# Kernel tuning notes

Hardware: AMD Instinct MI355X
Metric: run time of the kernel (lower is better)

## Reference

```python
import jax, jax.numpy as jnp
import numpy as np
from jax import lax

G = 64; ELL = 0.18; VOX = ELL / G
C_VIEWS = 6; H_IMG = 256; W_IMG = 256
MAX_N = 2048; PT = 0.25; MT = 0.25; FILL = 0.45
CHUNK = 256; RADIUS_CLIP = 2.0; NEAR = 0.01


def _rotz(a):
    c, s = jnp.cos(a), jnp.sin(a)
    z = jnp.zeros_like(c); o = jnp.ones_like(c)
    return jnp.stack([jnp.stack([c, -s, z]), jnp.stack([s, c, z]), jnp.stack([z, z, o])])


def _quat_to_mat4(q):
    # faithful replication of quaternion_matrix_torch_batch (incl. its asymmetries), fp32
    eps = 4 * np.finfo(np.float32).eps
    n = jnp.sum(q * q, 1)
    qs = q * jnp.sqrt(2.0 / jnp.where(n < eps, 1.0, n))[:, None]
    o = jnp.einsum('bi,bj->bij', qs, qs)
    one = jnp.ones_like(n); zero = jnp.zeros_like(n)
    row0 = jnp.stack([1.0 - o[:, 2, 2] - o[:, 3, 3], o[:, 1, 2] - o[:, 3, 0], o[:, 1, 3] + o[:, 2, 0], zero], 1)
    row1 = jnp.stack([o[:, 1, 2] - o[:, 3, 0], one, o[:, 2, 3] - o[:, 1, 0], zero], 1)
    row2 = jnp.stack([o[:, 1, 3] - o[:, 2, 0], o[:, 2, 3] + o[:, 1, 0], 1.0 - o[:, 1, 1] - o[:, 2, 2], zero], 1)
    row3 = jnp.stack([zero, zero, zero, one], 1)
    M = jnp.stack([row0, row1, row2, row3], 1)
    return jnp.where((n < eps)[:, None, None], jnp.eye(4, dtype=q.dtype), M)


def _quat_from_mat4(m):
    m00, m01, m02 = m[:, 0, 0], m[:, 0, 1], m[:, 0, 2]
    m10, m11, m12 = m[:, 1, 0], m[:, 1, 1], m[:, 1, 2]
    m20, m21, m22 = m[:, 2, 0], m[:, 2, 1], m[:, 2, 2]
    r0 = jnp.stack([m00 - m11 - m22, m01 + m10, m02 + m20, m21 - m12], 1)
    r1 = jnp.stack([m01 + m10, m11 - m00 - m22, m12 + m21, m02 - m20], 1)
    r2 = jnp.stack([m02 + m20, m12 + m21, m22 - m00 - m11, m10 - m01], 1)
    r3 = jnp.stack([m21 - m12, m02 - m20, m10 - m01, m00 + m11 + m22], 1)
    K = jnp.stack([r0, r1, r2, r3], 1) / 3.0
    _, V = jnp.linalg.eigh(K)
    q = V[:, :, -1][:, jnp.array([3, 0, 1, 2])]
    return jnp.where(q[:, :1] < 0.0, -q, q)


def _splat(means, quats, scales, opac, colors, viewmat, K, bg):
    R3, t3 = viewmat[:3, :3], viewmat[:3, 3]
    cam = means @ R3.T + t3
    x, y, z = cam[:, 0], cam[:, 1], cam[:, 2]
    fx, fy, cx, cy = K[0, 0], K[1, 1], K[0, 2], K[1, 2]
    qn = quats / (jnp.linalg.norm(quats, axis=1, keepdims=True) + 1e-12)
    w, qx, qy, qz = qn[:, 0], qn[:, 1], qn[:, 2], qn[:, 3]
    Rq = jnp.stack([
        jnp.stack([1 - 2 * (qy * qy + qz * qz), 2 * (qx * qy - w * qz), 2 * (qx * qz + w * qy)], 1),
        jnp.stack([2 * (qx * qy + w * qz), 1 - 2 * (qx * qx + qz * qz), 2 * (qy * qz - w * qx)], 1),
        jnp.stack([2 * (qx * qz - w * qy), 2 * (qy * qz + w * qx), 1 - 2 * (qx * qx + qy * qy)], 1)], 1)
    cov3 = jnp.einsum('nij,nj,nkj->nik', Rq, scales ** 2, Rq)
    covc = jnp.einsum('ij,njk,lk->nil', R3, cov3, R3)
    rz = 1.0 / z
    zn = jnp.zeros_like(z)
    J = jnp.stack([jnp.stack([fx * rz, zn, -fx * x * rz * rz], 1),
                   jnp.stack([zn, fy * rz, -fy * y * rz * rz], 1)], 1)  # [N,2,3]
    cov2 = jnp.einsum('nij,njk,nlk->nil', J, covc, J)
    a2 = cov2[:, 0, 0] + 0.3; b2 = cov2[:, 0, 1]; c2 = cov2[:, 1, 1] + 0.3  # gsplat screen dilation
    det = a2 * c2 - b2 * b2
    det_s = jnp.where(det > 1e-12, det, 1.0)
    ca = c2 / det_s; cb = -b2 / det_s; cc = a2 / det_s  # conic
    lam = 0.5 * (a2 + c2) + jnp.sqrt(jnp.maximum(0.25 * (a2 - c2) ** 2 + b2 * b2, 1e-12))
    radius = jnp.ceil(3.0 * jnp.sqrt(lam))
    mu_x = fx * x * rz + cx; mu_y = fy * y * rz + cy
    valid = (z > NEAR) & (det > 1e-12) & (radius > RADIUS_CLIP)
    op = jnp.where(valid, opac, 0.0)
    order = jnp.argsort(z)  # front-to-back
    gac = lambda a: a[order].reshape(-1, CHUNK, *a.shape[1:])
    chunks = (gac(mu_x), gac(mu_y), gac(ca), gac(cb), gac(cc), gac(op), gac(colors))
    xs = jnp.arange(W_IMG, dtype=means.dtype) + 0.5
    ys = jnp.arange(H_IMG, dtype=means.dtype) + 0.5

    @jax.checkpoint
    def body(carry, ch):
        rgb, T = carry
        ux, uy, A, B, Cc, o_, col = ch
        dx = xs[None, None, :] - ux[:, None, None]          # [c,1,W]->[c,H,W]
        dy = ys[None, :, None] - uy[:, None, None]
        sigma = 0.5 * (A[:, None, None] * dx * dx + Cc[:, None, None] * dy * dy) + B[:, None, None] * dx * dy
        alpha = o_[:, None, None] * jnp.exp(-sigma)
        alpha = jnp.where((sigma >= 0) & (alpha >= 1.0 / 255.0), jnp.minimum(alpha, 0.999), 0.0)
        cp = jnp.cumprod(1.0 - alpha, axis=0)
        Tin = jnp.concatenate([jnp.ones_like(cp[:1]), cp[:-1]], 0)  # exclusive transmittance in chunk
        wgt = alpha * Tin * T[None]
        rgb = rgb + jnp.einsum('nhw,nc->hwc', wgt, col)
        return (rgb, T * cp[-1]), None

    init = (jnp.zeros((H_IMG, W_IMG, 3), means.dtype), jnp.ones((H_IMG, W_IMG), means.dtype))
    (rgb, T), _ = lax.scan(body, init, chunks)
    alpha_img = 1.0 - T
    rgb = jnp.clip(rgb + T[..., None] * bg, 0.0, 1.0)
    return rgb[None], alpha_img[None, :, :, None]


def _forward(mask, img, p_3d, angle, grid, Ks, viewmats, w1, b1, w2, b2, scale_param, background, view_num):
    m = mask[0]; im = img[0]
    Rz = _rotz(angle)
    # ---- shape carving: project canonical grid into all views ----
    pw = grid @ Rz.T + p_3d                                   # [V,3]
    cam = jnp.einsum('cij,vj->cvi', viewmats[:, :3, :3], pw) + viewmats[:, None, :3, 3]
    z = cam[..., 2]
    proj = jnp.einsum('cij,cvj->cvi', Ks, cam)
    u = proj[..., 0] / z; v = proj[..., 1] / z
    ui = jnp.clip(jnp.round(u).astype(jnp.int32), 0, W_IMG - 1)
    vi = jnp.clip(jnp.round(v).astype(jnp.int32), 0, H_IMG - 1)
    inb = (u >= 0) & (u < W_IMG) & (v >= 0) & (v < H_IMG) & (z > NEAR)
    cidx = jnp.arange(C_VIEWS)[:, None]
    inside = inb & (m[cidx, vi, ui] > 0.5)
    csamp = im[cidx, vi, ui]                                  # [C,V,3]
    wv = inside.astype(grid.dtype)
    frac = wv.mean(0)
    col = (wv[..., None] * csamp).sum(0) / jnp.maximum(wv.sum(0), 1.0)[:, None]
    col = jnp.where((frac >= 1.0 - 1e-6)[:, None], col, FILL)
    volume = jnp.concatenate([10.0 * frac[None] - 5.0, col.T,
                              jnp.zeros((4, grid.shape[0]), grid.dtype)], 0)  # [8, G^3] (ablation pad)
    # ---- gaussian param extraction (static top-k instead of threshold search) ----
    probs = jax.nn.sigmoid(volume[0] - MT)
    _, idx = lax.top_k(probs, MAX_N)
    feats = volume[:, idx].T                                  # [N,8]
    h = jax.nn.relu(feats @ w1 + b1)
    out = h @ w2 + b2
    quats, scl, _op, cols, dmu = jnp.split(out, [4, 7, 8, 11], axis=1)
    colors = jnp.clip(jax.nn.sigmoid(cols), 0.0, 0.99)
    scales = jnp.exp(scl + scale_param[0])
    opac = jax.nn.sigmoid(jnp.clip((probs[idx] - PT) / (1.0 - PT), 0.0, 1.0))
    means = grid[idx] + 2.0 * VOX * jnp.tanh(dmu)
    # ---- pose transform ----
    means = means @ Rz.T + p_3d
    Rz4 = jnp.eye(4, dtype=means.dtype).at[:3, :3].set(Rz)
    r = jnp.einsum('ij,bjk->bik', Rz4, _quat_to_mat4(quats))
    quats = _quat_from_mat4(r)
    return _splat(means, quats, scales, opac, colors, viewmats[view_num], Ks[view_num], background)


def setup_inputs() -> dict:
    key = jax.random.key(0)
    ks = jax.random.split(key, 6)
    mask = jax.random.uniform(ks[0], (1, C_VIEWS, H_IMG, W_IMG), jnp.float32)
    img = jax.random.uniform(ks[1], (1, C_VIEWS, H_IMG, W_IMG, 3), jnp.float32)
    p_3d = jax.random.normal(ks[2], (3,), jnp.float32) * 0.02
    angle = jax.random.uniform(ks[3], (), jnp.float32) * 2.0 * np.pi
    lin = np.linspace(-ELL / 2, ELL / 2, G, dtype=np.float32)
    gx, gy, gz = np.meshgrid(lin, lin, lin, indexing='ij')
    grid = jnp.asarray(np.stack([gx, gy, gz], -1).reshape(-1, 3))
    Kmat = np.array([[300.0, 0.0, W_IMG / 2], [0.0, 300.0, H_IMG / 2], [0.0, 0.0, 1.0]], np.float32)
    Ks = jnp.asarray(np.stack([Kmat] * C_VIEWS))
    vms = []
    up = np.array([0.0, 0.0, 1.0])
    for i in range(C_VIEWS):
        th = 2 * np.pi * i / C_VIEWS
        eye = np.array([0.8 * np.cos(th), 0.8 * np.sin(th), 0.25])
        f = -eye / np.linalg.norm(eye)
        r = np.cross(f, up); r = r / np.linalg.norm(r)
        d = np.cross(f, r)
        vm = np.eye(4, dtype=np.float32)
        vm[:3, :3] = np.stack([r, d, f]).astype(np.float32)
        vm[:3, 3] = -vm[:3, :3] @ eye.astype(np.float32)
        vms.append(vm)
    viewmats = jnp.asarray(np.stack(vms))
    w1 = jax.random.normal(ks[4], (8, 128), jnp.float32) * 0.3
    b1 = jnp.zeros((128,), jnp.float32)
    w2 = jax.random.normal(ks[5], (128, 14), jnp.float32) * 0.2
    b2 = jnp.zeros((14,), jnp.float32)
    scale_param = jnp.full((1,), -5.5, jnp.float32)
    background = jnp.ones((3,), jnp.float32)
    return dict(mask=mask, img=img, p_3d=p_3d, angle=angle, grid=grid, Ks=Ks, viewmats=viewmats,
                w1=w1, b1=b1, w2=w2, b2=b2, scale_param=scale_param, background=background, view_num=0)


def reference(mask, img, p_3d, angle, grid, Ks, viewmats, w1, b1, w2, b2, scale_param, background, view_num):
    return _forward(mask, img, p_3d, angle, grid, Ks, viewmats, w1, b1, w2, b2, scale_param, background, view_num)
```

## Files before the change

kernel.cpp:

```cpp
#include <hip/hip_runtime.h>
#include <hip/hip_bf16.h>

namespace {
constexpr int GN   = 262144;
constexpr int CV   = 6;
constexpr int HI   = 256, WI = 256;
constexpr int MAXN = 2048;
constexpr int CBLK = 256;
constexpr int NSEG = 8;
constexpr float NEARZ = 0.01f;
constexpr float FILLC = 0.45f;

constexpr size_t OFF_CNT   = 0;
constexpr size_t OFF_BC8   = OFF_CNT + GN;
constexpr size_t OFF_SEL   = OFF_BC8 + CBLK*8*4;
constexpr size_t OFF_SCNT  = OFF_SEL + MAXN*4;
constexpr size_t OFF_PAR   = OFF_SCNT + MAXN*4;
constexpr size_t OFF_KEY   = OFF_PAR + MAXN*12*4;
constexpr size_t OFF_SPAR  = OFF_KEY + MAXN*8;
constexpr size_t OFF_PART  = OFF_SPAR + MAXN*12*4;
constexpr size_t WS_NEED   = OFF_PART + (size_t)256*NSEG*256*16;
}

__device__ __forceinline__ float sigm_(float x){ return 1.0f/(1.0f+expf(-x)); }

__global__ void __launch_bounds__(1024) k_count(
    const float* __restrict__ mask, const float* __restrict__ grid,
    const float* __restrict__ p3d, const float* __restrict__ angle,
    const float* __restrict__ Ks, const float* __restrict__ vms,
    unsigned char* __restrict__ cnt8, int* __restrict__ bc8)
{
  int t = threadIdx.x;
  int p = blockIdx.x*1024 + t;
  float a = angle[0];
  float ca = cosf(a), sa = sinf(a);
  float gx = grid[p*3+0], gy = grid[p*3+1], gz = grid[p*3+2];
  float pwx = ca*gx - sa*gy + p3d[0];
  float pwy = sa*gx + ca*gy + p3d[1];
  float pwz = gz + p3d[2];
  int count = 0;
  for (int c = 0; c < CV; ++c){
    const float* R = vms + c*16;
    float cxx = R[0]*pwx + R[1]*pwy + R[2]*pwz + R[3];
    float cyy = R[4]*pwx + R[5]*pwy + R[6]*pwz + R[7];
    float czz = R[8]*pwx + R[9]*pwy + R[10]*pwz + R[11];
    const float* K = Ks + c*9;
    float u = (K[0]*cxx + K[1]*cyy + K[2]*czz)/czz;
    float v = (K[3]*cxx + K[4]*cyy + K[5]*czz)/czz;
    bool inb = (u>=0.f)&&(u<(float)WI)&&(v>=0.f)&&(v<(float)HI)&&(czz>NEARZ);
    int ui = (int)fminf(fmaxf(rintf(u),0.f),(float)(WI-1));
    int vi = (int)fminf(fmaxf(rintf(v),0.f),(float)(HI-1));
    bool inside = inb && (mask[(c*HI+vi)*WI+ui] > 0.5f);
    count += inside ? 1 : 0;
  }
  cnt8[p] = (unsigned char)count;
  __shared__ int lh[8];
  if (t < 8) lh[t] = 0;
  __syncthreads();
  int L = 6 - count;
  unsigned long long msk[7];
  #pragma unroll
  for (int lv = 0; lv < 7; ++lv) msk[lv] = __ballot(L == lv);
  int lane = t & 63;
  if (lane < 7){
    int c = (int)__popcll(msk[lane]);
    if (c) atomicAdd(&lh[lane], c);
  }
  __syncthreads();
  if (t < 8) bc8[blockIdx.x*8 + t] = lh[t];
}

__global__ void __launch_bounds__(1024) k_select(const unsigned char* __restrict__ cnt8,
                                                 const int* __restrict__ bc8,
                                                 int* __restrict__ sel, int* __restrict__ scnt)
{
  int t = threadIdx.x, blk = blockIdx.x;
  __shared__ int sc[7][CBLK];
  if (t < CBLK){
    const int* row = bc8 + t*8;
    #pragma unroll
    for (int k = 0; k < 7; ++k) sc[k][t] = row[k];
  }
  __syncthreads();
  for (int ofs = 1; ofs < CBLK; ofs <<= 1){
    int x0 = 0, x1 = 0;
    int i0 = t & 255, L0 = t >> 8;
    int i1 = i0, L1 = L0 + 4;
    x0 = (i0 >= ofs) ? sc[L0][i0-ofs] : 0;
    if (L1 < 7) x1 = (i1 >= ofs) ? sc[L1][i1-ofs] : 0;
    __syncthreads();
    sc[L0][i0] += x0;
    if (L1 < 7) sc[L1][i1] += x1;
    __syncthreads();
  }
  __shared__ int pre[7], tot[7];
  if (t < 7){
    tot[t] = sc[t][CBLK-1];
    pre[t] = sc[t][blk] - bc8[blk*8 + t];
  }
  __syncthreads();
  int p = blk*1024 + t;
  int cnt = cnt8[p];
  int L = 6 - cnt;
  int lsL = 0;
  for (int l = 0; l < L; ++l) lsL += tot[l];
  unsigned long long msk[7];
  #pragma unroll
  for (int lv = 0; lv < 7; ++lv) msk[lv] = __ballot(L == lv);
  int lane = t & 63, wv = t >> 6;
  __shared__ int wcnt[16][7];
  if (lane < 7) wcnt[wv][lane] = (int)__popcll(msk[lane]);
  __syncthreads();
  int local = (int)__popcll(msk[L] & ((1ull<<lane)-1ull));
  for (int w = 0; w < wv; ++w) local += wcnt[w][L];
  int pos = lsL + pre[L] + local;
  if (pos < MAXN){ sel[pos] = p; scnt[pos] = cnt; }
}

#define JROT(dp,dq,opq, okp1,okq1, okp2,okq2, vp0,vq0,vp1,vq1,vp2,vq2,vp3,vq3)  \
  { float apq_ = opq;                                                           \
    if (fabsf(apq_) > 1e-30f){                                                  \
      float th_ = (dq - dp)/(2.f*apq_);                                         \
      float tt_ = (th_>=0.f?1.f:-1.f)/(fabsf(th_)+sqrtf(th_*th_+1.f));          \
      float c_ = 1.f/sqrtf(tt_*tt_+1.f), s_ = tt_*c_;                           \
      dp -= tt_*apq_; dq += tt_*apq_; opq = 0.f;                                \
      float t1_=okp1, t2_=okq1; okp1 = c_*t1_ - s_*t2_; okq1 = s_*t1_ + c_*t2_; \
      t1_=okp2; t2_=okq2; okp2 = c_*t1_ - s_*t2_; okq2 = s_*t1_ + c_*t2_;       \
      t1_=vp0; t2_=vq0; vp0 = c_*t1_ - s_*t2_; vq0 = s_*t1_ + c_*t2_;           \
      t1_=vp1; t2_=vq1; vp1 = c_*t1_ - s_*t2_; vq1 = s_*t1_ + c_*t2_;           \
      t1_=vp2; t2_=vq2; vp2 = c_*t1_ - s_*t2_; vq2 = s_*t1_ + c_*t2_;           \
      t1_=vp3; t2_=vq3; vp3 = c_*t1_ - s_*t2_; vq3 = s_*t1_ + c_*t2_;           \
    } }

__global__ void __launch_bounds__(64, 1) k_mlp_params(
    const float* __restrict__ mask, const float* __restrict__ img,
    const float* __restrict__ grid, const float* __restrict__ p3d,
    const float* __restrict__ angle, const float* __restrict__ Ks,
    const float* __restrict__ vms, const float* __restrict__ w1,
    const float* __restrict__ b1, const float* __restrict__ w2,
    const float* __restrict__ b2, const float* __restrict__ scp,
    const int* __restrict__ vnp, const int* __restrict__ sel,
    const int* __restrict__ scnt, float* __restrict__ par,
    unsigned long long* __restrict__ keys)
{
  __shared__ float4 w1t[128];
  __shared__ float4 w2t[128*4];
  __shared__ float  b1s[128];
  __shared__ float  b2s[16];
  int t = threadIdx.x;
  for (int j = t; j < 128; j += 64){
    w1t[j] = make_float4(w1[j], w1[128+j], w1[256+j], w1[384+j]);
    b1s[j] = b1[j];
  }
  {
    float* w2f = (float*)w2t;
    for (int i = t; i < 2048; i += 64){
      int j = i >> 4, c = i & 15;
      w2f[i] = (c < 14) ? w2[j*14+c] : 0.f;
    }
  }
  if (t < 14) b2s[t] = b2[t];
  else if (t < 16) b2s[t] = 0.f;
  __syncthreads();
  int s = blockIdx.x*64 + t;
  int p = sel[s];
  int cnt = scnt[s];
  float a = angle[0];
  float cA = cosf(a), sA = sinf(a);
  float gx = grid[p*3+0], gy = grid[p*3+1], gz = grid[p*3+2];
  float pwx = cA*gx - sA*gy + p3d[0];
  float pwy = sA*gx + cA*gy + p3d[1];
  float pwz = gz + p3d[2];
  float sr = 0.f, sg = 0.f, sb = 0.f;
  #pragma unroll
  for (int c = 0; c < CV; ++c){
    const float* R = vms + c*16;
    float cxx = R[0]*pwx + R[1]*pwy + R[2]*pwz + R[3];
    float cyy = R[4]*pwx + R[5]*pwy + R[6]*pwz + R[7];
    float czz = R[8]*pwx + R[9]*pwy + R[10]*pwz + R[11];
    const float* K = Ks + c*9;
    float u = (K[0]*cxx + K[1]*cyy + K[2]*czz)/czz;
    float v = (K[3]*cxx + K[4]*cyy + K[5]*czz)/czz;
    bool inb = (u>=0.f)&&(u<(float)WI)&&(v>=0.f)&&(v<(float)HI)&&(czz>NEARZ);
    int ui = (int)fminf(fmaxf(rintf(u),0.f),(float)(WI-1));
    int vi = (int)fminf(fmaxf(rintf(v),0.f),(float)(HI-1));
    bool inside = inb && (mask[(c*HI+vi)*WI+ui] > 0.5f);
    if (inside){
      const float* ip = img + ((size_t)(c*HI+vi)*WI+ui)*3;
      sr += ip[0]; sg += ip[1]; sb += ip[2];
    }
  }
  float f0 = 10.f*((float)cnt/6.f) - 5.f;
  float f1, f2, f3;
  if (cnt == 6){ f1 = sr/6.f; f2 = sg/6.f; f3 = sb/6.f; }
  else { f1 = FILLC; f2 = FILLC; f3 = FILLC; }
  float o0=b2s[0],o1=b2s[1],o2=b2s[2],o3=b2s[3],o4=b2s[4],o5=b2s[5],o6=b2s[6];
  float o7=b2s[7],o8=b2s[8],o9=b2s[9],o10=b2s[10],o11=b2s[11],o12=b2s[12],o13=b2s[13];
  #pragma unroll 4
  for (int j = 0; j < 128; ++j){
    float4 wv = w1t[j];
    float hj = b1s[j] + f0*wv.x + f1*wv.y + f2*wv.z + f3*wv.w;
    hj = fmaxf(hj, 0.f);
    float4 wa = w2t[j*4+0], wb = w2t[j*4+1], wc = w2t[j*4+2], wd = w2t[j*4+3];
    o0 += hj*wa.x;  o1 += hj*wa.y;  o2 += hj*wa.z;  o3 += hj*wa.w;
    o4 += hj*wb.x;  o5 += hj*wb.y;  o6 += hj*wb.z;  o7 += hj*wb.w;
    o8 += hj*wc.x;  o9 += hj*wc.y;  o10 += hj*wc.z; o11 += hj*wc.w;
    o12 += hj*wd.x; o13 += hj*wd.y;
  }
  float q0=o0, q1=o1, q2=o2, q3=o3;
  float nq = q0*q0+q1*q1+q2*q2+q3*q3;
  float M00,M01,M02,M10,M11,M12,M20,M21,M22;
  if (nq < 4.76837158e-07f){
    M00=1.f;M01=0.f;M02=0.f;M10=0.f;M11=1.f;M12=0.f;M20=0.f;M21=0.f;M22=1.f;
  } else {
    float s2 = 2.0f/nq;
    float e11=q1*q1*s2, e22=q2*q2*s2, e33=q3*q3*s2;
    float e12=q1*q2*s2, e13=q1*q3*s2, e23=q2*q3*s2;
    float e10=q1*q0*s2, e20=q2*q0*s2, e30=q3*q0*s2;
    M00=1.f-e22-e33; M01=e12-e30; M02=e13+e20;
    M10=e12-e30;     M11=1.f;     M12=e23-e10;
    M20=e13-e20;     M21=e23+e10; M22=1.f-e11-e22;
  }
  float r00 = cA*M00 - sA*M10, r01 = cA*M01 - sA*M11, r02 = cA*M02 - sA*M12;
  float r10 = sA*M00 + cA*M10, r11 = sA*M01 + cA*M11, r12 = sA*M02 + cA*M12;
  float r20 = M20, r21 = M21, r22 = M22;
  float d0=(r00-r11-r22)/3.f, d1=(r11-r00-r22)/3.f, d2=(r22-r00-r11)/3.f, d3=(r00+r11+r22)/3.f;
  float g01=(r01+r10)/3.f, g02=(r02+r20)/3.f, g03=(r21-r12)/3.f;
  float g12=(r12+r21)/3.f, g13=(r02-r20)/3.f, g23=(r10-r01)/3.f;
  float v00=1.f,v01=0.f,v02=0.f,v03=0.f;
  float v10=0.f,v11=1.f,v12=0.f,v13=0.f;
  float v20=0.f,v21=0.f,v22=1.f,v23=0.f;
  float v30=0.f,v31=0.f,v32=0.f,v33=1.f;
  for (int sweep = 0; sweep < 7; ++sweep){
    JROT(d0,d1,g01, g02,g12, g03,g13, v00,v01, v10,v11, v20,v21, v30,v31)
    JROT(d0,d2,g02, g01,g12, g03,g23, v00,v02, v10,v12, v20,v22, v30,v32)
    JROT(d0,d3,g03, g01,g13, g02,g23, v00,v03, v10,v13, v20,v23, v30,v33)
    JROT(d1,d2,g12, g01,g02, g13,g23, v01,v02, v11,v12, v21,v22, v31,v32)
    JROT(d1,d3,g13, g01,g03, g12,g23, v01,v03, v11,v13, v21,v23, v31,v33)
    JROT(d2,d3,g23, g02,g03, g12,g13, v02,v03, v12,v13, v22,v23, v32,v33)
  }
  float bv = d0, qw = v30, qx = v00, qy = v10, qz = v20;
  if (d1 > bv){ bv = d1; qw = v31; qx = v01; qy = v11; qz = v21; }
  if (d2 > bv){ bv = d2; qw = v32; qx = v02; qy = v12; qz = v22; }
  if (d3 > bv){ bv = d3; qw = v33; qx = v03; qy = v13; qz = v23; }
  float qlen = sqrtf(qw*qw+qx*qx+qy*qy+qz*qz) + 1e-12f;
  float w = qw/qlen, x = qx/qlen, y = qy/qlen, z = qz/qlen;
  float Rq00 = 1.f-2.f*(y*y+z*z), Rq01 = 2.f*(x*y - w*z), Rq02 = 2.f*(x*z + w*y);
  float Rq10 = 2.f*(x*y + w*z), Rq11 = 1.f-2.f*(x*x+z*z), Rq12 = 2.f*(y*z - w*x);
  float Rq20 = 2.f*(x*z - w*y), Rq21 = 2.f*(y*z + w*x), Rq22 = 1.f-2.f*(x*x+y*y);
  float spv = scp[0];
  float sc0 = expf(o4+spv), sc1 = expf(o5+spv), sc2 = expf(o6+spv);
  float va = sc0*sc0, vb = sc1*sc1, vc = sc2*sc2;
  float C300 = Rq00*Rq00*va + Rq01*Rq01*vb + Rq02*Rq02*vc;
  float C301 = Rq00*Rq10*va + Rq01*Rq11*vb + Rq02*Rq12*vc;
  float C302 = Rq00*Rq20*va + Rq01*Rq21*vb + Rq02*Rq22*vc;
  float C311 = Rq10*Rq10*va + Rq11*Rq11*vb + Rq12*Rq12*vc;
  float C312 = Rq10*Rq20*va + Rq11*Rq21*vb + Rq12*Rq22*vc;
  float C322 = Rq20*Rq20*va + Rq21*Rq21*vb + Rq22*Rq22*vc;
  const float TWOVOX = (float)(2.0*(0.18/64.0));
  float mlx = gx + TWOVOX*tanhf(o11);
  float mly = gy + TWOVOX*tanhf(o12);
  float mlz = gz + TWOVOX*tanhf(o13);
  float mx = cA*mlx - sA*mly + p3d[0];
  float my = sA*mlx + cA*mly + p3d[1];
  float mz = mlz + p3d[2];
  int vn = vnp[0];
  const float* vm = vms + vn*16;
  const float* Kc = Ks + vn*9;
  float xc = vm[0]*mx + vm[1]*my + vm[2]*mz + vm[3];
  float yc = vm[4]*mx + vm[5]*my + vm[6]*mz + vm[7];
  float zc = vm[8]*mx + vm[9]*my + vm[10]*mz + vm[11];
  float R0=vm[0], R1=vm[1], R2=vm[2], R4=vm[4], R5=vm[5], R6=vm[6], R8=vm[8], R9=vm[9], R10=vm[10];
  float T00 = R0*C300 + R1*C301 + R2*C302;
  float T01 = R0*C301 + R1*C311 + R2*C312;
  float T02 = R0*C302 + R1*C312 + R2*C322;
  float T10 = R4*C300 + R5*C301 + R6*C302;
  float T11 = R4*C301 + R5*C311 + R6*C312;
  float T12 = R4*C302 + R5*C312 + R6*C322;
  float T20 = R8*C300 + R9*C301 + R10*C302;
  float T21 = R8*C301 + R9*C311 + R10*C312;
  float T22 = R8*C302 + R9*C312 + R10*C322;
  float cc00 = T00*R0 + T01*R1 + T02*R2;
  float cc01 = T00*R4 + T01*R5 + T02*R6;
  float cc02 = T00*R8 + T01*R9 + T02*R10;
  float cc11 = T10*R4 + T11*R5 + T12*R6;
  float cc12 = T10*R8 + T11*R9 + T12*R10;
  float cc22 = T20*R8 + T21*R9 + T22*R10;
  float fx = Kc[0], fy = Kc[4], cxk = Kc[2], cyk = Kc[5];
  float rz = 1.f/zc;
  float jx0 = fx*rz, jx2 = -fx*xc*rz*rz;
  float jy1 = fy*rz, jy2 = -fy*yc*rz*rz;
  float c2_00 = jx0*jx0*cc00 + 2.f*jx0*jx2*cc02 + jx2*jx2*cc22;
  float c2_01 = jx0*jy1*cc01 + jx0*jy2*cc02 + jx2*jy1*cc12 + jx2*jy2*cc22;
  float c2_11 = jy1*jy1*cc11 + 2.f*jy1*jy2*cc12 + jy2*jy2*cc22;
  float a2 = c2_00 + 0.3f, b2v = c2_01, c2 = c2_11 + 0.3f;
  float det = a2*c2 - b2v*b2v;
  float dets = (det > 1e-12f) ? det : 1.f;
  float conA = c2/dets, conB = -b2v/dets, conC = a2/dets;
  float lam = 0.5f*(a2+c2) + sqrtf(fmaxf(0.25f*(a2-c2)*(a2-c2) + b2v*b2v, 1e-12f));
  float radius = ceilf(3.f*sqrtf(lam));
  float mux = fx*xc*rz + cxk, muy = fy*yc*rz + cyk;
  bool valid = (zc > NEARZ) && (det > 1e-12f) && (radius > 2.0f);
  float prob = sigm_(10.f*((float)cnt/6.f) - 5.f - 0.25f);
  float t01 = fminf(fmaxf((prob - 0.25f)/0.75f, 0.f), 1.f);
  float opac = sigm_(t01);
  float op = valid ? opac : 0.f;
  float colr = fminf(fmaxf(sigm_(o8), 0.f), 0.99f);
  float colg = fminf(fmaxf(sigm_(o9), 0.f), 0.99f);
  float colb = fminf(fmaxf(sigm_(o10), 0.f), 0.99f);
  float tln = (op > 0.f) ? logf(255.f*op) : 0.f;
  float rxp = sqrtf(fmaxf(2.f*tln*a2, 0.f)) + 1.0f;
  float ryp = sqrtf(fmaxf(2.f*tln*c2, 0.f)) + 1.0f;
  float* pr = par + s*12;
  pr[0]=mux; pr[1]=muy; pr[2]=conA; pr[3]=conB; pr[4]=conC;
  pr[5]=op; pr[6]=colr; pr[7]=colg; pr[8]=colb; pr[9]=zc;
  pr[10] = valid ? rxp : -1e9f;
  pr[11] = valid ? ryp : -1e9f;
  unsigned int zb = __float_as_uint(zc);
  zb = (zb & 0x80000000u) ? ~zb : (zb | 0x80000000u);
  keys[s] = ((unsigned long long)zb << 11) | (unsigned long long)s;
}

__global__ void __launch_bounds__(1024) k_ranksort(const unsigned long long* __restrict__ keys,
                                                   const float* __restrict__ par,
                                                   float* __restrict__ spar)
{
  __shared__ unsigned long long kk[MAXN];
  __shared__ int pc[8][128];
  __shared__ int rk[128];
  int t = threadIdx.x;
  kk[t] = keys[t]; kk[t+1024] = keys[t+1024];
  int iloc = t & 127, jseg = t >> 7;
  int i = blockIdx.x*128 + iloc;
  unsigned long long ki = keys[i];
  __syncthreads();
  int cnt = 0;
  const int j0 = jseg*256;
  #pragma unroll 8
  for (int n = 0; n < 256; ++n) cnt += (kk[j0+n] < ki) ? 1 : 0;
  pc[jseg][iloc] = cnt;
  __syncthreads();
  if (t < 128){
    int r = 0;
    #pragma unroll
    for (int sgi = 0; sgi < 8; ++sgi) r += pc[sgi][t];
    rk[t] = r;
  }
  __syncthreads();
  for (int idx = t; idx < 128*12; idx += 1024){
    int row = idx/12, q = idx - row*12;
    spar[(size_t)rk[row]*12 + q] = par[(size_t)(blockIdx.x*128 + row)*12 + q];
  }
}

__global__ void __launch_bounds__(256) k_raster_part(const float* __restrict__ spar,
                                                     float4* __restrict__ part)
{
  int raw = blockIdx.x;
  int seg = raw & (NSEG-1);
  int tilep = raw >> 3;
  int tile = (tilep*97 + seg*31) & 255;
  int tx = tile & 15, ty = tile >> 4;
  int lx = threadIdx.x & 15, ly = threadIdx.x >> 4;
  float pxc = tx*16 + lx + 0.5f, pyc = ty*16 + ly + 0.5f;
  float tileX0 = tx*16 + 0.5f, tileX1 = tx*16 + 15.5f;
  float tileY0 = ty*16 + 0.5f, tileY1 = ty*16 + 15.5f;
  __shared__ float lp[256*9];
  __shared__ int wbase[4];
  int lane = threadIdx.x & 63, wv = threadIdx.x >> 6;
  const float* gp = spar + (size_t)(seg*256 + threadIdx.x)*12;
  float mux = gp[0], muy = gp[1], op = gp[5], rx = gp[10], ry = gp[11];
  bool keep = (op > 0.f) &&
              (mux + rx >= tileX0) && (mux - rx <= tileX1) &&
              (muy + ry >= tileY0) && (muy - ry <= tileY1);
  unsigned long long m = __ballot(keep);
  if (lane == 0) wbase[wv] = (int)__popcll(m);
  __syncthreads();
  int base = 0, total = 0;
  #pragma unroll
  for (int w = 0; w < 4; ++w){ if (w < wv) base += wbase[w]; total += wbase[w]; }
  if (keep){
    int pos = base + (int)__popcll(m & ((1ull<<lane)-1ull));
    float* dst = lp + pos*9;
    dst[0]=mux; dst[1]=muy; dst[2]=gp[2]; dst[3]=gp[3]; dst[4]=gp[4];
    dst[5]=op;  dst[6]=gp[6]; dst[7]=gp[7]; dst[8]=gp[8];
  }
  __syncthreads();
  float T = 1.f, rr = 0.f, gg = 0.f, bb = 0.f;
  for (int n = 0; n < total; ++n){
    const float* g = lp + n*9;
    float dx = pxc - g[0], dy = pyc - g[1];
    float sig = 0.5f*(g[2]*dx*dx + g[4]*dy*dy) + g[3]*dx*dy;
    float alpha = g[5]*expf(-sig);
    if (sig >= 0.f && alpha >= 1.0f/255.0f){
      alpha = fminf(alpha, 0.999f);
      float wgt = alpha*T;
      rr += wgt*g[6]; gg += wgt*g[7]; bb += wgt*g[8];
      T *= (1.f - alpha);
    }
  }
  part[(size_t)(tile*NSEG + seg)*256 + threadIdx.x] = make_float4(rr, gg, bb, T);
}

__global__ void __launch_bounds__(256) k_combine(const float4* __restrict__ part,
                                                 const float* __restrict__ bg,
                                                 float* __restrict__ outp)
{
  int tile = blockIdx.x;
  int t = threadIdx.x;
  int tx = tile & 15, ty = tile >> 4;
  int px = tx*16 + (t & 15), py = ty*16 + (t >> 4);
  float rr = 0.f, gg = 0.f, bb = 0.f, T = 1.f;
  #pragma unroll
  for (int seg = 0; seg < NSEG; ++seg){
    float4 v = part[(size_t)(tile*NSEG + seg)*256 + t];
    rr += T*v.x; gg += T*v.y; bb += T*v.z; T *= v.w;
  }
  int pix = py*WI + px;
  outp[pix*3+0] = fminf(fmaxf(rr + T*bg[0], 0.f), 1.f);
  outp[pix*3+1] = fminf(fmaxf(gg + T*bg[1], 0.f), 1.f);
  outp[pix*3+2] = fminf(fmaxf(bb + T*bg[2], 0.f), 1.f);
  outp[HI*WI*3 + pix] = 1.f - T;
}

__global__ void __launch_bounds__(256) k_raster_mono(const float* __restrict__ spar,
                                                     const float* __restrict__ bg,
                                                     float* __restrict__ outp)
{
  int tile = blockIdx.x;
  int tx = tile & 15, ty = tile >> 4;
  int lx = threadIdx.x & 15, ly = threadIdx.x >> 4;
  int px = tx*16 + lx, py = ty*16 + ly;
  float pxc = px + 0.5f, pyc = py + 0.5f;
  float tileX0 = tx*16 + 0.5f, tileX1 = tx*16 + 15.5f;
  float tileY0 = ty*16 + 0.5f, tileY1 = ty*16 + 15.5f;
  float T = 1.f, rr = 0.f, gg = 0.f, bb = 0.f;
  __shared__ float lp[256*9];
  __shared__ int wbase[4];
  int lane = threadIdx.x & 63, wv = threadIdx.x >> 6;
  for (int ch = 0; ch < MAXN; ch += 256){
    const float* gp = spar + (size_t)(ch + threadIdx.x)*12;
    float mux = gp[0], muy = gp[1], op = gp[5], rx = gp[10], ry = gp[11];
    bool keep = (op > 0.f) &&
                (mux + rx >= tileX0) && (mux - rx <= tileX1) &&
                (muy + ry >= tileY0) && (muy - ry <= tileY1);
    unsigned long long m = __ballot(keep);
    int wc = (int)__popcll(m);
    __syncthreads();
    if (lane == 0) wbase[wv] = wc;
    __syncthreads();
    int base = 0, total = 0;
    #pragma unroll
    for (int w = 0; w < 4; ++w){ if (w < wv) base += wbase[w]; total += wbase[w]; }
    if (keep){
      int pos = base + (int)__popcll(m & ((1ull<<lane)-1ull));
      float* dst = lp + pos*9;
      dst[0]=mux; dst[1]=muy; dst[2]=gp[2]; dst[3]=gp[3]; dst[4]=gp[4];
      dst[5]=op;  dst[6]=gp[6]; dst[7]=gp[7]; dst[8]=gp[8];
    }
    __syncthreads();
    for (int n = 0; n < total; ++n){
      const float* g = lp + n*9;
      float dx = pxc - g[0], dy = pyc - g[1];
      float sig = 0.5f*(g[2]*dx*dx + g[4]*dy*dy) + g[3]*dx*dy;
      float alpha = g[5]*expf(-sig);
      if (sig >= 0.f && alpha >= 1.0f/255.0f){
        alpha = fminf(alpha, 0.999f);
        float wgt = alpha*T;
        rr += wgt*g[6]; gg += wgt*g[7]; bb += wgt*g[8];
        T *= (1.f - alpha);
      }
    }
  }
  int pix = py*WI + px;
  outp[pix*3+0] = fminf(fmaxf(rr + T*bg[0], 0.f), 1.f);
  outp[pix*3+1] = fminf(fmaxf(gg + T*bg[1], 0.f), 1.f);
  outp[pix*3+2] = fminf(fmaxf(bb + T*bg[2], 0.f), 1.f);
  outp[HI*WI*3 + pix] = 1.f - T;
}

extern "C" void kernel_launch(void* const* d_in, const int* in_sizes, int n_in,
                              void* d_out, int out_size, void* d_ws, size_t ws_size,
                              hipStream_t stream)
{
  const float* mask  = (const float*)d_in[0];
  const float* img   = (const float*)d_in[1];
  const float* p3d   = (const float*)d_in[2];
  const float* angle = (const float*)d_in[3];
  const float* grid  = (const float*)d_in[4];
  const float* Ks    = (const float*)d_in[5];
  const float* vms   = (const float*)d_in[6];
  const float* w1    = (const float*)d_in[7];
  const float* b1    = (const float*)d_in[8];
  const float* w2    = (const float*)d_in[9];
  const float* b2    = (const float*)d_in[10];
  const float* scp   = (const float*)d_in[11];
  const float* bg    = (const float*)d_in[12];
  const int*   vn    = (const int*)d_in[13];
  float* outp = (float*)d_out;
  char* ws = (char*)d_ws;
  unsigned char* cnt8 = (unsigned char*)(ws + OFF_CNT);
  int* bc8   = (int*)(ws + OFF_BC8);
  int* sel   = (int*)(ws + OFF_SEL);
  int* scnt  = (int*)(ws + OFF_SCNT);
  float* par   = (float*)(ws + OFF_PAR);
  unsigned long long* keys = (unsigned long long*)(ws + OFF_KEY);
  float* spar  = (float*)(ws + OFF_SPAR);
  float4* part = (float4*)(ws + OFF_PART);

  k_count     <<<CBLK, 1024, 0, stream>>>(mask, grid, p3d, angle, Ks, vms, cnt8, bc8);
  k_select    <<<CBLK, 1024, 0, stream>>>(cnt8, bc8, sel, scnt);
  k_mlp_params<<<MAXN/64, 64, 0, stream>>>(mask, img, grid, p3d, angle, Ks, vms,
                                           w1, b1, w2, b2, scp, vn, sel, scnt, par, keys);
  k_ranksort  <<<MAXN/128, 1024, 0, stream>>>(keys, par, spar);
  if (ws_size >= WS_NEED){
    k_raster_part<<<256*NSEG, 256, 0, stream>>>(spar, part);
    k_combine    <<<256, 256, 0, stream>>>(part, bg, outp);
  } else {
    k_raster_mono<<<256, 256, 0, stream>>>(spar, bg, outp);
  }
}
```

Baseline: 169.2 us.

## Assign one wavefront per selected point in MLP param kernel

k_mlp_params now gives each selected Gaussian a full 64-lane wavefront instead of one thread. The six view projections are spread across lanes, and the 128 hidden units are split two per lane. Partial sums are combined with xor-shuffle reductions, and lane 0 writes the outputs. This replaces a 32-block grid of serial per-thread loops with 512 blocks of highly parallel work and drops the shared-memory weight staging. The cost is redundant per-lane computation of the eigen/covariance tail and 17 wave reductions.

```diff
diff --git a/kernel.cpp b/kernel.cpp
--- a/kernel.cpp
+++ b/kernel.cpp
@@ -23,6 +23,11 @@
 }
 
 __device__ __forceinline__ float sigm_(float x){ return 1.0f/(1.0f+expf(-x)); }
+__device__ __forceinline__ float wsum_(float v){
+  v += __shfl_xor(v, 32, 64); v += __shfl_xor(v, 16, 64); v += __shfl_xor(v, 8, 64);
+  v += __shfl_xor(v, 4, 64);  v += __shfl_xor(v, 2, 64);  v += __shfl_xor(v, 1, 64);
+  return v;
+}
 
 __global__ void __launch_bounds__(1024) k_count(
     const float* __restrict__ mask, const float* __restrict__ grid,
@@ -132,7 +137,7 @@
       t1_=vp3; t2_=vq3; vp3 = c_*t1_ - s_*t2_; vq3 = s_*t1_ + c_*t2_;           \
     } }
 
-__global__ void __launch_bounds__(64, 1) k_mlp_params(
+__global__ void __launch_bounds__(256) k_mlp_params(
     const float* __restrict__ mask, const float* __restrict__ img,
     const float* __restrict__ grid, const float* __restrict__ p3d,
     const float* __restrict__ angle, const float* __restrict__ Ks,
@@ -143,70 +148,57 @@
     const int* __restrict__ scnt, float* __restrict__ par,
     unsigned long long* __restrict__ keys)
 {
-  __shared__ float4 w1t[128];
-  __shared__ float4 w2t[128*4];
-  __shared__ float  b1s[128];
-  __shared__ float  b2s[16];
-  int t = threadIdx.x;
-  for (int j = t; j < 128; j += 64){
-    w1t[j] = make_float4(w1[j], w1[128+j], w1[256+j], w1[384+j]);
-    b1s[j] = b1[j];
-  }
-  {
-    float* w2f = (float*)w2t;
-    for (int i = t; i < 2048; i += 64){
-      int j = i >> 4, c = i & 15;
-      w2f[i] = (c < 14) ? w2[j*14+c] : 0.f;
-    }
-  }
-  if (t < 14) b2s[t] = b2[t];
-  else if (t < 16) b2s[t] = 0.f;
-  __syncthreads();
-  int s = blockIdx.x*64 + t;
+  int lane = threadIdx.x & 63, wvi = threadIdx.x >> 6;
+  int s = blockIdx.x*4 + wvi;
   int p = sel[s];
   int cnt = scnt[s];
   float a = angle[0];
   float cA = cosf(a), sA = sinf(a);
   float gx = grid[p*3+0], gy = grid[p*3+1], gz = grid[p*3+2];
-  float pwx = cA*gx - sA*gy + p3d[0];
-  float pwy = sA*gx + cA*gy + p3d[1];
-  float pwz = gz + p3d[2];
   float sr = 0.f, sg = 0.f, sb = 0.f;
-  #pragma unroll
-  for (int c = 0; c < CV; ++c){
-    const float* R = vms + c*16;
+  if (lane < 6){
+    float pwx = cA*gx - sA*gy + p3d[0];
+    float pwy = sA*gx + cA*gy + p3d[1];
+    float pwz = gz + p3d[2];
+    const float* R = vms + lane*16;
     float cxx = R[0]*pwx + R[1]*pwy + R[2]*pwz + R[3];
     float cyy = R[4]*pwx + R[5]*pwy + R[6]*pwz + R[7];
     float czz = R[8]*pwx + R[9]*pwy + R[10]*pwz + R[11];
-    const float* K = Ks + c*9;
+    const float* K = Ks + lane*9;
     float u = (K[0]*cxx + K[1]*cyy + K[2]*czz)/czz;
     float v = (K[3]*cxx + K[4]*cyy + K[5]*czz)/czz;
     bool inb = (u>=0.f)&&(u<(float)WI)&&(v>=0.f)&&(v<(float)HI)&&(czz>NEARZ);
     int ui = (int)fminf(fmaxf(rintf(u),0.f),(float)(WI-1));
     int vi = (int)fminf(fmaxf(rintf(v),0.f),(float)(HI-1));
-    bool inside = inb && (mask[(c*HI+vi)*WI+ui] > 0.5f);
+    bool inside = inb && (mask[(lane*HI+vi)*WI+ui] > 0.5f);
     if (inside){
-      const float* ip = img + ((size_t)(c*HI+vi)*WI+ui)*3;
-      sr += ip[0]; sg += ip[1]; sb += ip[2];
+      const float* ip = img + ((size_t)(lane*HI+vi)*WI+ui)*3;
+      sr = ip[0]; sg = ip[1]; sb = ip[2];
     }
   }
+  sr = wsum_(sr); sg = wsum_(sg); sb = wsum_(sb);
   float f0 = 10.f*((float)cnt/6.f) - 5.f;
   float f1, f2, f3;
   if (cnt == 6){ f1 = sr/6.f; f2 = sg/6.f; f3 = sb/6.f; }
   else { f1 = FILLC; f2 = FILLC; f3 = FILLC; }
-  float o0=b2s[0],o1=b2s[1],o2=b2s[2],o3=b2s[3],o4=b2s[4],o5=b2s[5],o6=b2s[6];
-  float o7=b2s[7],o8=b2s[8],o9=b2s[9],o10=b2s[10],o11=b2s[11],o12=b2s[12],o13=b2s[13];
-  #pragma unroll 4
-  for (int j = 0; j < 128; ++j){
-    float4 wv = w1t[j];
-    float hj = b1s[j] + f0*wv.x + f1*wv.y + f2*wv.z + f3*wv.w;
+  float o0=0.f,o1=0.f,o2=0.f,o3=0.f,o4=0.f,o5=0.f,o6=0.f;
+  float o7=0.f,o8=0.f,o9=0.f,o10=0.f,o11=0.f,o12=0.f,o13=0.f;
+  #pragma unroll
+  for (int r = 0; r < 2; ++r){
+    int j = lane + r*64;
+    float hj = b1[j] + f0*w1[j] + f1*w1[128+j] + f2*w1[256+j] + f3*w1[384+j];
     hj = fmaxf(hj, 0.f);
-    float4 wa = w2t[j*4+0], wb = w2t[j*4+1], wc = w2t[j*4+2], wd = w2t[j*4+3];
-    o0 += hj*wa.x;  o1 += hj*wa.y;  o2 += hj*wa.z;  o3 += hj*wa.w;
-    o4 += hj*wb.x;  o5 += hj*wb.y;  o6 += hj*wb.z;  o7 += hj*wb.w;
-    o8 += hj*wc.x;  o9 += hj*wc.y;  o10 += hj*wc.z; o11 += hj*wc.w;
-    o12 += hj*wd.x; o13 += hj*wd.y;
-  }
+    const float* w2r = w2 + j*14;
+    o0 += hj*w2r[0];  o1 += hj*w2r[1];  o2 += hj*w2r[2];  o3 += hj*w2r[3];
+    o4 += hj*w2r[4];  o5 += hj*w2r[5];  o6 += hj*w2r[6];  o7 += hj*w2r[7];
+    o8 += hj*w2r[8];  o9 += hj*w2r[9];  o10 += hj*w2r[10]; o11 += hj*w2r[11];
+    o12 += hj*w2r[12]; o13 += hj*w2r[13];
+  }
+  o0 = wsum_(o0) + b2[0];   o1 = wsum_(o1) + b2[1];   o2 = wsum_(o2) + b2[2];
+  o3 = wsum_(o3) + b2[3];   o4 = wsum_(o4) + b2[4];   o5 = wsum_(o5) + b2[5];
+  o6 = wsum_(o6) + b2[6];   o7 = wsum_(o7) + b2[7];   o8 = wsum_(o8) + b2[8];
+  o9 = wsum_(o9) + b2[9];   o10 = wsum_(o10) + b2[10]; o11 = wsum_(o11) + b2[11];
+  o12 = wsum_(o12) + b2[12]; o13 = wsum_(o13) + b2[13];
   float q0=o0, q1=o1, q2=o2, q3=o3;
   float nq = q0*q0+q1*q1+q2*q2+q3*q3;
   float M00,M01,M02,M10,M11,M12,M20,M21,M22;
@@ -311,14 +303,16 @@
   float tln = (op > 0.f) ? logf(255.f*op) : 0.f;
   float rxp = sqrtf(fmaxf(2.f*tln*a2, 0.f)) + 1.0f;
   float ryp = sqrtf(fmaxf(2.f*tln*c2, 0.f)) + 1.0f;
-  float* pr = par + s*12;
-  pr[0]=mux; pr[1]=muy; pr[2]=conA; pr[3]=conB; pr[4]=conC;
-  pr[5]=op; pr[6]=colr; pr[7]=colg; pr[8]=colb; pr[9]=zc;
-  pr[10] = valid ? rxp : -1e9f;
-  pr[11] = valid ? ryp : -1e9f;
-  unsigned int zb = __float_as_uint(zc);
-  zb = (zb & 0x80000000u) ? ~zb : (zb | 0x80000000u);
-  keys[s] = ((unsigned long long)zb << 11) | (unsigned long long)s;
+  if (lane == 0){
+    float* pr = par + s*12;
+    pr[0]=mux; pr[1]=muy; pr[2]=conA; pr[3]=conB; pr[4]=conC;
+    pr[5]=op; pr[6]=colr; pr[7]=colg; pr[8]=colb; pr[9]=zc;
+    pr[10] = valid ? rxp : -1e9f;
+    pr[11] = valid ? ryp : -1e9f;
+    unsigned int zb = __float_as_uint(zc);
+    zb = (zb & 0x80000000u) ? ~zb : (zb | 0x80000000u);
+    keys[s] = ((unsigned long long)zb << 11) | (unsigned long long)s;
+  }
 }
 
 __global__ void __launch_bounds__(1024) k_ranksort(const unsigned long long* __restrict__ keys,
@@ -510,7 +504,7 @@
 
   k_count     <<<CBLK, 1024, 0, stream>>>(mask, grid, p3d, angle, Ks, vms, cnt8, bc8);
   k_select    <<<CBLK, 1024, 0, stream>>>(cnt8, bc8, sel, scnt);
-  k_mlp_params<<<MAXN/64, 64, 0, stream>>>(mask, img, grid, p3d, angle, Ks, vms,
+  k_mlp_params<<<MAXN/4, 256, 0, stream>>>(mask, img, grid, p3d, angle, Ks, vms,
                                            w1, b1, w2, b2, scp, vn, sel, scnt, par, keys);
   k_ranksort  <<<MAXN/128, 1024, 0, stream>>>(keys, par, spar);
   if (ws_size >= WS_NEED){
```

Result: faster. 155.3 us (-8.2%).

## Fuse selection scan into MLP parameter kernel and vectorize Gaussian records

Applied to the files above, without the earlier changes.

Merges the compaction/select kernel with the MLP/parameter kernel, so each selected voxel's thread computes its parameters directly and the sel/scnt round-trip and one launch go away. Parameter records are written and copied as float4, and the rasterizers stage them in shared memory as two float4 arrays plus one float. The trade-off is that each 1024-thread block now reloads the MLP weights and runs the prefix scan, and selected threads are spread unevenly across 256 blocks with reduced occupancy from the larger register footprint.

```diff
diff --git a/kernel.cpp b/kernel.cpp
--- a/kernel.cpp
+++ b/kernel.cpp
@@ -13,9 +13,7 @@
 
 constexpr size_t OFF_CNT   = 0;
 constexpr size_t OFF_BC8   = OFF_CNT + GN;
-constexpr size_t OFF_SEL   = OFF_BC8 + CBLK*8*4;
-constexpr size_t OFF_SCNT  = OFF_SEL + MAXN*4;
-constexpr size_t OFF_PAR   = OFF_SCNT + MAXN*4;
+constexpr size_t OFF_PAR   = OFF_BC8 + CBLK*8*4;
 constexpr size_t OFF_KEY   = OFF_PAR + MAXN*12*4;
 constexpr size_t OFF_SPAR  = OFF_KEY + MAXN*8;
 constexpr size_t OFF_PART  = OFF_SPAR + MAXN*12*4;
@@ -70,53 +68,6 @@
   if (t < 8) bc8[blockIdx.x*8 + t] = lh[t];
 }
 
-__global__ void __launch_bounds__(1024) k_select(const unsigned char* __restrict__ cnt8,
-                                                 const int* __restrict__ bc8,
-                                                 int* __restrict__ sel, int* __restrict__ scnt)
-{
-  int t = threadIdx.x, blk = blockIdx.x;
-  __shared__ int sc[7][CBLK];
-  if (t < CBLK){
-    const int* row = bc8 + t*8;
-    #pragma unroll
-    for (int k = 0; k < 7; ++k) sc[k][t] = row[k];
-  }
-  __syncthreads();
-  for (int ofs = 1; ofs < CBLK; ofs <<= 1){
-    int x0 = 0, x1 = 0;
-    int i0 = t & 255, L0 = t >> 8;
-    int i1 = i0, L1 = L0 + 4;
-    x0 = (i0 >= ofs) ? sc[L0][i0-ofs] : 0;
-    if (L1 < 7) x1 = (i1 >= ofs) ? sc[L1][i1-ofs] : 0;
-    __syncthreads();
-    sc[L0][i0] += x0;
-    if (L1 < 7) sc[L1][i1] += x1;
-    __syncthreads();
-  }
-  __shared__ int pre[7], tot[7];
-  if (t < 7){
-    tot[t] = sc[t][CBLK-1];
-    pre[t] = sc[t][blk] - bc8[blk*8 + t];
-  }
-  __syncthreads();
-  int p = blk*1024 + t;
-  int cnt = cnt8[p];
-  int L = 6 - cnt;
-  int lsL = 0;
-  for (int l = 0; l < L; ++l) lsL += tot[l];
-  unsigned long long msk[7];
-  #pragma unroll
-  for (int lv = 0; lv < 7; ++lv) msk[lv] = __ballot(L == lv);
-  int lane = t & 63, wv = t >> 6;
-  __shared__ int wcnt[16][7];
-  if (lane < 7) wcnt[wv][lane] = (int)__popcll(msk[lane]);
-  __syncthreads();
-  int local = (int)__popcll(msk[L] & ((1ull<<lane)-1ull));
-  for (int w = 0; w < wv; ++w) local += wcnt[w][L];
-  int pos = lsL + pre[L] + local;
-  if (pos < MAXN){ sel[pos] = p; scnt[pos] = cnt; }
-}
-
 #define JROT(dp,dq,opq, okp1,okq1, okp2,okq2, vp0,vq0,vp1,vq1,vp2,vq2,vp3,vq3)  \
   { float apq_ = opq;                                                           \
     if (fabsf(apq_) > 1e-30f){                                                  \
@@ -132,39 +83,78 @@
       t1_=vp3; t2_=vq3; vp3 = c_*t1_ - s_*t2_; vq3 = s_*t1_ + c_*t2_;           \
     } }
 
-__global__ void __launch_bounds__(64, 1) k_mlp_params(
+__global__ void __launch_bounds__(1024) k_select_mlp(
+    const unsigned char* __restrict__ cnt8, const int* __restrict__ bc8,
     const float* __restrict__ mask, const float* __restrict__ img,
     const float* __restrict__ grid, const float* __restrict__ p3d,
     const float* __restrict__ angle, const float* __restrict__ Ks,
     const float* __restrict__ vms, const float* __restrict__ w1,
     const float* __restrict__ b1, const float* __restrict__ w2,
     const float* __restrict__ b2, const float* __restrict__ scp,
-    const int* __restrict__ vnp, const int* __restrict__ sel,
-    const int* __restrict__ scnt, float* __restrict__ par,
+    const int* __restrict__ vnp, float* __restrict__ par,
     unsigned long long* __restrict__ keys)
 {
+  int t = threadIdx.x, blk = blockIdx.x;
+  __shared__ int sc[7][CBLK];
   __shared__ float4 w1t[128];
   __shared__ float4 w2t[128*4];
   __shared__ float  b1s[128];
   __shared__ float  b2s[16];
-  int t = threadIdx.x;
-  for (int j = t; j < 128; j += 64){
+  if (t < CBLK){
+    const int* row = bc8 + t*8;
+    #pragma unroll
+    for (int k = 0; k < 7; ++k) sc[k][t] = row[k];
+  } else if (t < CBLK + 128){
+    int j = t - CBLK;
     w1t[j] = make_float4(w1[j], w1[128+j], w1[256+j], w1[384+j]);
     b1s[j] = b1[j];
-  }
-  {
+  } else if (t < CBLK + 128 + 16){
+    int j = t - CBLK - 128;
+    b2s[j] = (j < 14) ? b2[j] : 0.f;
+  }
+  if (t >= 512){
     float* w2f = (float*)w2t;
-    for (int i = t; i < 2048; i += 64){
-      int j = i >> 4, c = i & 15;
+    int base = (t - 512)*4;
+    #pragma unroll
+    for (int q = 0; q < 4; ++q){
+      int i = base + q; int j = i >> 4, c = i & 15;
       w2f[i] = (c < 14) ? w2[j*14+c] : 0.f;
     }
   }
-  if (t < 14) b2s[t] = b2[t];
-  else if (t < 16) b2s[t] = 0.f;
-  __syncthreads();
-  int s = blockIdx.x*64 + t;
-  int p = sel[s];
-  int cnt = scnt[s];
+  __syncthreads();
+  for (int ofs = 1; ofs < CBLK; ofs <<= 1){
+    int x0 = 0, x1 = 0;
+    int i0 = t & 255, L0 = t >> 8;
+    int i1 = i0, L1 = L0 + 4;
+    x0 = (i0 >= ofs) ? sc[L0][i0-ofs] : 0;
+    if (L1 < 7) x1 = (i1 >= ofs) ? sc[L1][i1-ofs] : 0;
+    __syncthreads();
+    sc[L0][i0] += x0;
+    if (L1 < 7) sc[L1][i1] += x1;
+    __syncthreads();
+  }
+  __shared__ int pre[7], tot[7];
+  if (t < 7){
+    tot[t] = sc[t][CBLK-1];
+    pre[t] = sc[t][blk] - bc8[blk*8 + t];
+  }
+  __syncthreads();
+  int p = blk*1024 + t;
+  int cnt = cnt8[p];
+  int L = 6 - cnt;
+  int lsL = 0;
+  for (int l = 0; l < L; ++l) lsL += tot[l];
+  unsigned long long msk[7];
+  #pragma unroll
+  for (int lv = 0; lv < 7; ++lv) msk[lv] = __ballot(L == lv);
+  int lane = t & 63, wv = t >> 6;
+  __shared__ int wcnt[16][7];
+  if (lane < 7) wcnt[wv][lane] = (int)__popcll(msk[lane]);
+  __syncthreads();
+  int local = (int)__popcll(msk[L] & ((1ull<<lane)-1ull));
+  for (int w = 0; w < wv; ++w) local += wcnt[w][L];
+  int pos = lsL + pre[L] + local;
+  if (pos >= MAXN) return;
   float a = angle[0];
   float cA = cosf(a), sA = sinf(a);
   float gx = grid[p*3+0], gy = grid[p*3+1], gz = grid[p*3+2];
@@ -198,8 +188,8 @@
   float o7=b2s[7],o8=b2s[8],o9=b2s[9],o10=b2s[10],o11=b2s[11],o12=b2s[12],o13=b2s[13];
   #pragma unroll 4
   for (int j = 0; j < 128; ++j){
-    float4 wv = w1t[j];
-    float hj = b1s[j] + f0*wv.x + f1*wv.y + f2*wv.z + f3*wv.w;
+    float4 wv4 = w1t[j];
+    float hj = b1s[j] + f0*wv4.x + f1*wv4.y + f2*wv4.z + f3*wv4.w;
     hj = fmaxf(hj, 0.f);
     float4 wa = w2t[j*4+0], wb = w2t[j*4+1], wc = w2t[j*4+2], wd = w2t[j*4+3];
     o0 += hj*wa.x;  o1 += hj*wa.y;  o2 += hj*wa.z;  o3 += hj*wa.w;
@@ -311,14 +301,13 @@
   float tln = (op > 0.f) ? logf(255.f*op) : 0.f;
   float rxp = sqrtf(fmaxf(2.f*tln*a2, 0.f)) + 1.0f;
   float ryp = sqrtf(fmaxf(2.f*tln*c2, 0.f)) + 1.0f;
-  float* pr = par + s*12;
-  pr[0]=mux; pr[1]=muy; pr[2]=conA; pr[3]=conB; pr[4]=conC;
-  pr[5]=op; pr[6]=colr; pr[7]=colg; pr[8]=colb; pr[9]=zc;
-  pr[10] = valid ? rxp : -1e9f;
-  pr[11] = valid ? ryp : -1e9f;
+  float4* pr4 = (float4*)(par + (size_t)pos*12);
+  pr4[0] = make_float4(mux, muy, conA, conB);
+  pr4[1] = make_float4(conC, op, colr, colg);
+  pr4[2] = make_float4(colb, zc, valid ? rxp : -1e9f, valid ? ryp : -1e9f);
   unsigned int zb = __float_as_uint(zc);
   zb = (zb & 0x80000000u) ? ~zb : (zb | 0x80000000u);
-  keys[s] = ((unsigned long long)zb << 11) | (unsigned long long)s;
+  keys[pos] = ((unsigned long long)zb << 11) | (unsigned long long)pos;
 }
 
 __global__ void __launch_bounds__(1024) k_ranksort(const unsigned long long* __restrict__ keys,
@@ -347,9 +336,11 @@
     rk[t] = r;
   }
   __syncthreads();
-  for (int idx = t; idx < 128*12; idx += 1024){
-    int row = idx/12, q = idx - row*12;
-    spar[(size_t)rk[row]*12 + q] = par[(size_t)(blockIdx.x*128 + row)*12 + q];
+  const float4* src4 = (const float4*)par;
+  float4* dst4 = (float4*)spar;
+  for (int idx = t; idx < 128*3; idx += 1024){
+    int row = idx/3, q = idx - row*3;
+    dst4[(size_t)rk[row]*3 + q] = src4[(size_t)(blockIdx.x*128 + row)*3 + q];
   }
 }
 
@@ -365,11 +356,16 @@
   float pxc = tx*16 + lx + 0.5f, pyc = ty*16 + ly + 0.5f;
   float tileX0 = tx*16 + 0.5f, tileX1 = tx*16 + 15.5f;
   float tileY0 = ty*16 + 0.5f, tileY1 = ty*16 + 15.5f;
-  __shared__ float lp[256*9];
+  __shared__ float4 lpA[256];
+  __shared__ float4 lpB[256];
+  __shared__ float  lpC[256];
   __shared__ int wbase[4];
   int lane = threadIdx.x & 63, wv = threadIdx.x >> 6;
-  const float* gp = spar + (size_t)(seg*256 + threadIdx.x)*12;
-  float mux = gp[0], muy = gp[1], op = gp[5], rx = gp[10], ry = gp[11];
+  const float4* sp4 = (const float4*)spar;
+  float4 v0 = sp4[(size_t)(seg*256 + threadIdx.x)*3 + 0];
+  float4 v1 = sp4[(size_t)(seg*256 + threadIdx.x)*3 + 1];
+  float4 v2 = sp4[(size_t)(seg*256 + threadIdx.x)*3 + 2];
+  float mux = v0.x, muy = v0.y, op = v1.y, rx = v2.z, ry = v2.w;
   bool keep = (op > 0.f) &&
               (mux + rx >= tileX0) && (mux - rx <= tileX1) &&
               (muy + ry >= tileY0) && (muy - ry <= tileY1);
@@ -381,21 +377,19 @@
   for (int w = 0; w < 4; ++w){ if (w < wv) base += wbase[w]; total += wbase[w]; }
   if (keep){
     int pos = base + (int)__popcll(m & ((1ull<<lane)-1ull));
-    float* dst = lp + pos*9;
-    dst[0]=mux; dst[1]=muy; dst[2]=gp[2]; dst[3]=gp[3]; dst[4]=gp[4];
-    dst[5]=op;  dst[6]=gp[6]; dst[7]=gp[7]; dst[8]=gp[8];
+    lpA[pos] = v0; lpB[pos] = v1; lpC[pos] = v2.x;
   }
   __syncthreads();
   float T = 1.f, rr = 0.f, gg = 0.f, bb = 0.f;
   for (int n = 0; n < total; ++n){
-    const float* g = lp + n*9;
-    float dx = pxc - g[0], dy = pyc - g[1];
-    float sig = 0.5f*(g[2]*dx*dx + g[4]*dy*dy) + g[3]*dx*dy;
-    float alpha = g[5]*expf(-sig);
+    float4 A = lpA[n], B = lpB[n];
+    float dx = pxc - A.x, dy = pyc - A.y;
+    float sig = 0.5f*(A.z*dx*dx + B.x*dy*dy) + A.w*dx*dy;
+    float alpha = B.y*expf(-sig);
     if (sig >= 0.f && alpha >= 1.0f/255.0f){
       alpha = fminf(alpha, 0.999f);
       float wgt = alpha*T;
-      rr += wgt*g[6]; gg += wgt*g[7]; bb += wgt*g[8];
+      rr += wgt*B.z; gg += wgt*B.w; bb += wgt*lpC[n];
       T *= (1.f - alpha);
     }
   }
@@ -435,12 +429,17 @@
   float tileX0 = tx*16 + 0.5f, tileX1 = tx*16 + 15.5f;
   float tileY0 = ty*16 + 0.5f, tileY1 = ty*16 + 15.5f;
   float T = 1.f, rr = 0.f, gg = 0.f, bb = 0.f;
-  __shared__ float lp[256*9];
+  __shared__ float4 lpA[256];
+  __shared__ float4 lpB[256];
+  __shared__ float  lpC[256];
   __shared__ int wbase[4];
   int lane = threadIdx.x & 63, wv = threadIdx.x >> 6;
+  const float4* sp4 = (const float4*)spar;
   for (int ch = 0; ch < MAXN; ch += 256){
-    const float* gp = spar + (size_t)(ch + threadIdx.x)*12;
-    float mux = gp[0], muy = gp[1], op = gp[5], rx = gp[10], ry = gp[11];
+    float4 v0 = sp4[(size_t)(ch + threadIdx.x)*3 + 0];
+    float4 v1 = sp4[(size_t)(ch + threadIdx.x)*3 + 1];
+    float4 v2 = sp4[(size_t)(ch + threadIdx.x)*3 + 2];
+    float mux = v0.x, muy = v0.y, op = v1.y, rx = v2.z, ry = v2.w;
     bool keep = (op > 0.f) &&
                 (mux + rx >= tileX0) && (mux - rx <= tileX1) &&
                 (muy + ry >= tileY0) && (muy - ry <= tileY1);
@@ -454,20 +453,18 @@
     for (int w = 0; w < 4; ++w){ if (w < wv) base += wbase[w]; total += wbase[w]; }
     if (keep){
       int pos = base + (int)__popcll(m & ((1ull<<lane)-1ull));
-      float* dst = lp + pos*9;
-      dst[0]=mux; dst[1]=muy; dst[2]=gp[2]; dst[3]=gp[3]; dst[4]=gp[4];
-      dst[5]=op;  dst[6]=gp[6]; dst[7]=gp[7]; dst[8]=gp[8];
+      lpA[pos] = v0; lpB[pos] = v1; lpC[pos] = v2.x;
     }
     __syncthreads();
     for (int n = 0; n < total; ++n){
-      const float* g = lp + n*9;
-      float dx = pxc - g[0], dy = pyc - g[1];
-      float sig = 0.5f*(g[2]*dx*dx + g[4]*dy*dy) + g[3]*dx*dy;
-      float alpha = g[5]*expf(-sig);
+      float4 A = lpA[n], B = lpB[n];
+      float dx = pxc - A.x, dy = pyc - A.y;
+      float sig = 0.5f*(A.z*dx*dx + B.x*dy*dy) + A.w*dx*dy;
+      float alpha = B.y*expf(-sig);
       if (sig >= 0.f && alpha >= 1.0f/255.0f){
         alpha = fminf(alpha, 0.999f);
         float wgt = alpha*T;
-        rr += wgt*g[6]; gg += wgt*g[7]; bb += wgt*g[8];
+        rr += wgt*B.z; gg += wgt*B.w; bb += wgt*lpC[n];
         T *= (1.f - alpha);
       }
     }
@@ -501,17 +498,14 @@
   char* ws = (char*)d_ws;
   unsigned char* cnt8 = (unsigned char*)(ws + OFF_CNT);
   int* bc8   = (int*)(ws + OFF_BC8);
-  int* sel   = (int*)(ws + OFF_SEL);
-  int* scnt  = (int*)(ws + OFF_SCNT);
   float* par   = (float*)(ws + OFF_PAR);
   unsigned long long* keys = (unsigned long long*)(ws + OFF_KEY);
   float* spar  = (float*)(ws + OFF_SPAR);
   float4* part = (float4*)(ws + OFF_PART);
 
   k_count     <<<CBLK, 1024, 0, stream>>>(mask, grid, p3d, angle, Ks, vms, cnt8, bc8);
-  k_select    <<<CBLK, 1024, 0, stream>>>(cnt8, bc8, sel, scnt);
-  k_mlp_params<<<MAXN/64, 64, 0, stream>>>(mask, img, grid, p3d, angle, Ks, vms,
-                                           w1, b1, w2, b2, scp, vn, sel, scnt, par, keys);
+  k_select_mlp<<<CBLK, 1024, 0, stream>>>(cnt8, bc8, mask, img, grid, p3d, angle, Ks, vms,
+                                          w1, b1, w2, b2, scp, vn, par, keys);
   k_ranksort  <<<MAXN/128, 1024, 0, stream>>>(keys, par, spar);
   if (ws_size >= WS_NEED){
     k_raster_part<<<256*NSEG, 256, 0, stream>>>(spar, part);
```

Measured after the change: 214.0 us. 26.5% more time.
